# Kernel optimization log

Measured on AMD Instinct MI355X. Metric: run time of the kernel, lower is better.

The kernel has to match this reference:

```python
import jax, jax.numpy as jnp
import numpy as np
from jax import lax

DN = ('NCHW', 'OIHW', 'NCHW')
NUM_HEADS = 6


def _conv1x1(x, w):
    return lax.conv_general_dilated(x, w, (1, 1), 'VALID', dimension_numbers=DN)


def _dwconv3x3(x, w):
    # depthwise 3x3, groups == channels, padding 1
    return lax.conv_general_dilated(x, w, (1, 1), ((1, 1), (1, 1)),
                                    dimension_numbers=DN,
                                    feature_group_count=w.shape[0])


def setup_inputs() -> dict:
    key = jax.random.key(0)
    ks = jax.random.split(key, 7)
    b, dim, h, w = 4, 192, 128, 128
    inp = {
        'x': jax.random.normal(ks[0], (b, dim, h, w), jnp.float32),
        'ref': jax.random.normal(ks[1], (b, dim, h, w), jnp.float32),
        'w_qkv': jax.random.normal(ks[2], (dim * 3, dim, 1, 1), jnp.float32) * 0.05,
        'w_dw': jax.random.normal(ks[3], (dim * 3, 1, 3, 3), jnp.float32) * 0.1,
        'w_proj': jax.random.normal(ks[4], (dim, dim, 1, 1), jnp.float32) * 0.05,
        'temperature': jnp.ones((NUM_HEADS, 1, 1), jnp.float32),
        'attn_w': 0.2 * jnp.ones((4,), jnp.float32),
    }
    return inp


def reference(x, ref, w_qkv, w_dw, w_proj, temperature, attn_w):
    b, c, h, w = x.shape
    heads = NUM_HEADS
    C = c // heads  # per-head channel dim
    hw = h * w

    qkv = _dwconv3x3(_conv1x1(x, w_qkv), w_dw)        # [b, 3c, h, w]
    ref_qkv = _dwconv3x3(_conv1x1(ref, w_qkv), w_dw)  # shared weights

    q_shared = qkv[:, :c]            # q from x
    k_shared = ref_qkv[:, c:2 * c]   # k from ref
    v_shared = ref_qkv[:, 2 * c:]    # v from ref

    def to_heads(t):  # [b, c, h, w] -> [b, head, C, hw]
        return t.reshape(b, heads, C, hw)

    q = to_heads(q_shared)
    k = to_heads(k_shared)
    v = to_heads(v_shared)

    # L2-normalize along token dim (last axis)
    q = q / jnp.maximum(jnp.linalg.norm(q, axis=-1, keepdims=True), 1e-12)
    k = k / jnp.maximum(jnp.linalg.norm(k, axis=-1, keepdims=True), 1e-12)

    # channel-wise attention: [b, head, C, C]
    attn = jnp.einsum('bhcn,bhdn->bhcd', q, k) * temperature

    ks_list = [int(C / 2), int(C * 2 / 3), int(C * 3 / 4), int(C * 4 / 5)]
    neg_inf = jnp.asarray(-jnp.inf, attn.dtype)

    out = 0.0
    for i, ki in enumerate(ks_list):
        vals = lax.top_k(attn, ki)[0]            # [b, head, C, ki]
        thr = vals[..., -1:]                     # k-th largest per row
        a = jnp.where(attn >= thr, attn, neg_inf)
        a = jax.nn.softmax(a, axis=-1)
        out = out + attn_w[i] * jnp.einsum('bhcd,bhdn->bhcn', a, v)

    out = out.reshape(b, c, h, w)
    return _conv1x1(out, w_proj)
```

## Files before the change

kernel.cpp:

```cpp
#include <hip/hip_runtime.h>
#include <cstdint>
#include <cstddef>

typedef unsigned short u16;
typedef unsigned int u32;
typedef __attribute__((ext_vector_type(2))) float f32x2;
typedef __attribute__((ext_vector_type(4))) float f32x4;
typedef __attribute__((ext_vector_type(8))) short short8;
typedef __attribute__((ext_vector_type(2))) u32 u32x2;
typedef __attribute__((ext_vector_type(4))) u32 u32x4;

#define DEV static __device__ __forceinline__
#define HW 16384

DEV u16 f2bf(float f) {
  u32 u = __float_as_uint(f);
  u = (u + 0x7fffu + ((u >> 16) & 1u)) >> 16;
  return (u16)u;
}
DEV float bf2f(u16 h) { return __uint_as_float(((u32)h) << 16); }

DEV u32 packsplit(float f) {
  u16 h = f2bf(f);
  u16 l = f2bf(f - bf2f(h));
  return (u32)h | ((u32)l << 16);
}
DEV void unpack8(const u32* w, short8& hi, short8& lo) {
  #pragma unroll
  for (int i = 0; i < 8; ++i) {
    hi[i] = (short)(u16)w[i];
    lo[i] = (short)(u16)(w[i] >> 16);
  }
}
DEV void split8(const float* p, short8& hi, short8& lo) {
  f32x4 v0 = *(const f32x4*)p;
  f32x4 v1 = *(const f32x4*)(p + 4);
  #pragma unroll
  for (int j = 0; j < 4; ++j) {
    u16 h0 = f2bf(v0[j]);
    hi[j] = (short)h0; lo[j] = (short)f2bf(v0[j] - bf2f(h0));
    u16 h1 = f2bf(v1[j]);
    hi[4 + j] = (short)h1; lo[4 + j] = (short)f2bf(v1[j] - bf2f(h1));
  }
}
DEV void mfma3(f32x4& acc, short8 ah, short8 al, short8 bh, short8 bl) {
  acc = __builtin_amdgcn_mfma_f32_16x16x32_bf16(ah, bh, acc, 0, 0, 0);
  acc = __builtin_amdgcn_mfma_f32_16x16x32_bf16(ah, bl, acc, 0, 0, 0);
  acc = __builtin_amdgcn_mfma_f32_16x16x32_bf16(al, bh, acc, 0, 0, 0);
}

__global__ __launch_bounds__(256) void ksplit(const float* __restrict__ in,
                                              u32* __restrict__ out, int n) {
  int i = blockIdx.x * 256 + threadIdx.x;
  if (i < n) out[i] = packsplit(in[i]);
}

template<int ABATCH>
__global__ __launch_bounds__(512, 4) void gemm2(const u32* __restrict__ Asp,
                                                const float* __restrict__ B,
                                                float* __restrict__ C) {
  __shared__ u32 As[192 * 34];
  __shared__ u32 Bs[64 * 34];
  const int t = threadIdx.x, lane = t & 63, wid = t >> 6;
  const int b = blockIdx.z, n0 = blockIdx.x * 64;
  const u32* Ab = ABATCH ? (Asp + (size_t)b * 192 * 192) : Asp;
  const float* Bb = B + (size_t)b * 192 * (size_t)HW;
  float* Cb = C + (size_t)b * 192 * (size_t)HW;
  const int wr = wid >> 2, wc = wid & 3;
  const int g = lane >> 4, r16 = lane & 15;
  const int b_n = (t & 15) * 4, b_k = t >> 4;
  f32x4 acc[6] = {};

  f32x4 Breg, Bnext;
  u32x4 Areg[3];
  Breg = *(const f32x4*)&Bb[(size_t)b_k * HW + n0 + b_n];
  #pragma unroll
  for (int i = 0; i < 3; ++i) {
    int vi = t + i * 512;
    Areg[i] = *(const u32x4*)&Ab[(size_t)(vi >> 3) * 192 + ((vi & 7) << 2)];
  }
  #pragma unroll 1
  for (int p = 0; p < 6; ++p) {
    #pragma unroll
    for (int j = 0; j < 4; ++j)
      Bs[(b_n + j) * 34 + b_k] = packsplit(Breg[j]);
    #pragma unroll
    for (int i = 0; i < 3; ++i) {
      int vi = t + i * 512;
      int row = vi >> 3, kc = (vi & 7) << 2;
      u32x2 v0 = {Areg[i][0], Areg[i][1]};
      u32x2 v1 = {Areg[i][2], Areg[i][3]};
      *(u32x2*)&As[row * 34 + kc] = v0;
      *(u32x2*)&As[row * 34 + kc + 2] = v1;
    }
    if (p < 5)
      Bnext = *(const f32x4*)&Bb[(size_t)((p + 1) * 32 + b_k) * HW + n0 + b_n];
    __syncthreads();
    if (p < 5) {
      #pragma unroll
      for (int i = 0; i < 3; ++i) {
        int vi = t + i * 512;
        Areg[i] = *(const u32x4*)&Ab[(size_t)(vi >> 3) * 192 + (p + 1) * 32 + ((vi & 7) << 2)];
      }
    }
    u32 bw[8];
    {
      const u32* bp = &Bs[(wc * 16 + r16) * 34 + g * 8];
      *(u32x2*)&bw[0] = *(const u32x2*)&bp[0];
      *(u32x2*)&bw[2] = *(const u32x2*)&bp[2];
      *(u32x2*)&bw[4] = *(const u32x2*)&bp[4];
      *(u32x2*)&bw[6] = *(const u32x2*)&bp[6];
    }
    short8 bh, bl; unpack8(bw, bh, bl);
    #pragma unroll
    for (int mf = 0; mf < 6; ++mf) {
      u32 aw[8];
      const u32* ap = &As[(wr * 96 + mf * 16 + r16) * 34 + g * 8];
      *(u32x2*)&aw[0] = *(const u32x2*)&ap[0];
      *(u32x2*)&aw[2] = *(const u32x2*)&ap[2];
      *(u32x2*)&aw[4] = *(const u32x2*)&ap[4];
      *(u32x2*)&aw[6] = *(const u32x2*)&ap[6];
      short8 ah, al; unpack8(aw, ah, al);
      acc[mf] = __builtin_amdgcn_mfma_f32_16x16x32_bf16(ah, bh, acc[mf], 0, 0, 0);
      acc[mf] = __builtin_amdgcn_mfma_f32_16x16x32_bf16(ah, bl, acc[mf], 0, 0, 0);
      acc[mf] = __builtin_amdgcn_mfma_f32_16x16x32_bf16(al, bh, acc[mf], 0, 0, 0);
    }
    __syncthreads();
    Breg = Bnext;
  }
  #pragma unroll
  for (int mf = 0; mf < 6; ++mf)
    #pragma unroll
    for (int rr = 0; rr < 4; ++rr)
      Cb[(size_t)(wr * 96 + mf * 16 + g * 4 + rr) * HW + n0 + wc * 16 + r16] =
          acc[mf][rr];
}

template<int SSQ>
__global__ __launch_bounds__(512) void k2_dw(const float* __restrict__ Tin,
                                             const float* __restrict__ wdw, int wco,
                                             float* __restrict__ O,
                                             float* __restrict__ ssq, int sspath) {
  const int rt = blockIdx.x, cg = blockIdx.y, b = blockIdx.z;
  const int t = threadIdx.x, lane = t & 63, w = t >> 6;
  __shared__ float In[8][10][132];
  for (int idx = t; idx < 10400; idx += 512) {
    int ch = idx / 1300, rem = idx % 1300;
    int r = rem / 130, ci = rem % 130;
    int gr = rt * 8 + r - 1, gc = ci - 1;
    float v = 0.f;
    if (gr >= 0 && gr < 128 && gc >= 0 && gc < 128)
      v = Tin[((size_t)b * 192 + cg * 8 + ch) * HW + gr * 128 + gc];
    In[ch][r][ci] = v;
  }
  float wv[9];
  #pragma unroll
  for (int j = 0; j < 9; ++j) wv[j] = wdw[(size_t)(wco + cg * 8 + w) * 9 + j];
  __syncthreads();
  float s = 0.f;
  float* Op = O + ((size_t)b * 192 + cg * 8 + w) * HW + rt * 8 * 128 + 2 * lane;
  #pragma unroll
  for (int i = 0; i < 8; ++i) {
    float a0 = 0.f, a1 = 0.f;
    #pragma unroll
    for (int dr = 0; dr < 3; ++dr) {
      f32x2 u0 = *(const f32x2*)&In[w][i + dr][2 * lane];
      f32x2 u1 = *(const f32x2*)&In[w][i + dr][2 * lane + 2];
      a0 += wv[dr * 3] * u0[0] + wv[dr * 3 + 1] * u0[1] + wv[dr * 3 + 2] * u1[0];
      a1 += wv[dr * 3] * u0[1] + wv[dr * 3 + 1] * u1[0] + wv[dr * 3 + 2] * u1[1];
    }
    f32x2 o = {a0, a1};
    *(f32x2*)&Op[(size_t)i * 128] = o;
    if (SSQ) s += a0 * a0 + a1 * a1;
  }
  if (SSQ) {
    #pragma unroll
    for (int off = 32; off; off >>= 1) s += __shfl_down(s, off);
    if (lane == 0) ssq[(((size_t)b * 2 + sspath) * 192 + cg * 8 + w) * 16 + rt] = s;
  }
}

__global__ __launch_bounds__(256) void k3_gram(const float* __restrict__ q,
                                               const float* __restrict__ k,
                                               float* __restrict__ gp) {
  const int ck = blockIdx.x, bh = blockIdx.y;
  const int b = bh / 6, h = bh % 6;
  const int t = threadIdx.x, lane = t & 63, wid = t >> 6;
  const int r16 = lane & 15, g = lane >> 4;
  const int chunk = ck * 4 + wid;
  const size_t rbase = ((size_t)b * 192 + h * 32 + r16) * HW;
  const float* qp = q + rbase;
  const float* kp = k + rbase;
  f32x4 acc[2][2] = {};
  #pragma unroll 1
  for (int s = 0; s < 8; ++s) {
    int n = chunk * 256 + s * 32 + g * 8;
    short8 a0h, a0l, a1h, a1l, b0h, b0l, b1h, b1l;
    split8(&qp[n], a0h, a0l);
    split8(&qp[(size_t)16 * HW + n], a1h, a1l);
    split8(&kp[n], b0h, b0l);
    split8(&kp[(size_t)16 * HW + n], b1h, b1l);
    mfma3(acc[0][0], a0h, a0l, b0h, b0l);
    mfma3(acc[0][1], a0h, a0l, b1h, b1l);
    mfma3(acc[1][0], a1h, a1l, b0h, b0l);
    mfma3(acc[1][1], a1h, a1l, b1h, b1l);
  }
  float* outp = gp + ((size_t)bh * 64 + chunk) * 1024;
  #pragma unroll
  for (int mf = 0; mf < 2; ++mf)
    #pragma unroll
    for (int nf = 0; nf < 2; ++nf)
      #pragma unroll
      for (int rr = 0; rr < 4; ++rr)
        outp[(mf * 16 + g * 4 + rr) * 32 + nf * 16 + r16] = acc[mf][nf][rr];
}

__global__ __launch_bounds__(256) void k4_comb(const float* __restrict__ gp,
                                               const float* __restrict__ ssq,
                                               const float* __restrict__ temp,
                                               const float* __restrict__ aw,
                                               const float* __restrict__ wproj,
                                               float* __restrict__ mc) {
  const int bh = blockIdx.x, b = bh / 6, h = bh % 6;
  const int t = threadIdx.x;
  __shared__ float Gs[1024];
  __shared__ float Acm[1024];
  __shared__ float nq[32], nk[32];
  for (int e = t; e < 1024; e += 256) {
    const float* p = gp + ((size_t)bh * 64) * 1024 + e;
    float s = 0.f;
    for (int ch = 0; ch < 64; ++ch) s += p[(size_t)ch * 1024];
    Gs[e] = s;
  }
  if (t < 64) {
    int c = t & 31, pk = t >> 5;
    const float* sp = ssq + (((size_t)b * 2 + pk) * 192 + h * 32 + c) * 16;
    float s = 0.f;
    #pragma unroll
    for (int i = 0; i < 16; ++i) s += sp[i];
    float nr = fmaxf(sqrtf(s), 1e-12f);
    if (pk == 0) nq[c] = nr; else nk[c] = nr;
  }
  __syncthreads();
  const float T = temp[h];
  for (int e = t; e < 1024; e += 256) {
    int c = e >> 5, d = e & 31;
    Gs[e] = Gs[e] * T / (nq[c] * nk[d]);
  }
  __syncthreads();
  const float aw0 = aw[0], aw1 = aw[1], aw2 = aw[2], aw3 = aw[3];
  const int half = t >> 5, d = t & 31;
  for (int it = 0; it < 4; ++it) {
    const int c = it * 8 + half;
    const float v = Gs[c * 32 + d];
    int cnt = 0;
    #pragma unroll
    for (int dd = 0; dd < 32; ++dd) cnt += (Gs[c * 32 + dd] >= v) ? 1 : 0;
    float c0 = v;
    float c1 = (cnt >= 16) ? v : -3.0e38f;
    float c2 = (cnt >= 21) ? v : -3.0e38f;
    float c3 = (cnt >= 24) ? v : -3.0e38f;
    float c4 = (cnt >= 25) ? v : -3.0e38f;
    #pragma unroll
    for (int off = 16; off; off >>= 1) {
      c0 = fmaxf(c0, __shfl_xor(c0, off));
      c1 = fmaxf(c1, __shfl_xor(c1, off));
      c2 = fmaxf(c2, __shfl_xor(c2, off));
      c3 = fmaxf(c3, __shfl_xor(c3, off));
      c4 = fmaxf(c4, __shfl_xor(c4, off));
    }
    const float m = c0;
    const float ex = expf(v - m);
    float z1 = (v >= c1) ? ex : 0.f;
    float z2 = (v >= c2) ? ex : 0.f;
    float z3 = (v >= c3) ? ex : 0.f;
    float z4 = (v >= c4) ? ex : 0.f;
    #pragma unroll
    for (int off = 16; off; off >>= 1) {
      z1 += __shfl_xor(z1, off);
      z2 += __shfl_xor(z2, off);
      z3 += __shfl_xor(z3, off);
      z4 += __shfl_xor(z4, off);
    }
    float a = 0.f;
    a += (v >= c1) ? aw0 * ex / z1 : 0.f;
    a += (v >= c2) ? aw1 * ex / z2 : 0.f;
    a += (v >= c3) ? aw2 * ex / z3 : 0.f;
    a += (v >= c4) ? aw3 * ex / z4 : 0.f;
    Acm[c * 32 + d] = a;
  }
  __syncthreads();
  for (int idx = t; idx < 192 * 32; idx += 256) {
    int co = idx >> 5, dd = idx & 31;
    const float* wp = wproj + (size_t)co * 192 + h * 32;
    float s = 0.f;
    #pragma unroll
    for (int c = 0; c < 32; ++c) s += wp[c] * Acm[c * 32 + dd];
    mc[((size_t)b * 192 + co) * 192 + h * 32 + dd] = s;
  }
}

extern "C" void kernel_launch(void* const* d_in, const int* in_sizes, int n_in,
                              void* d_out, int out_size, void* d_ws, size_t ws_size,
                              hipStream_t stream) {
  const float* x     = (const float*)d_in[0];
  const float* ref   = (const float*)d_in[1];
  const float* wqkv  = (const float*)d_in[2];
  const float* wdw   = (const float*)d_in[3];
  const float* wproj = (const float*)d_in[4];
  const float* temp  = (const float*)d_in[5];
  const float* aw    = (const float*)d_in[6];
  float* out = (float*)d_out;
  char* ws = (char*)d_ws;

  const size_t S = (size_t)4 * 192 * HW * 4;
  float* tA  = (float*)(ws);
  float* tB  = (float*)(ws + S);
  float* qb  = (float*)(ws + 2 * S);
  float* kb  = (float*)(ws + 3 * S);
  float* gp  = (float*)(ws + 4 * S);
  float* ssq = (float*)(ws + 4 * S + 6291456);
  float* mc  = (float*)(ws + 4 * S + 6291456 + 98304);
  u32*   wsp = (u32*)(ws + 4 * S + 6291456 + 98304 + 589824);
  u32*   mcp = (u32*)(ws + 4 * S + 6291456 + 98304 + 589824 + 442368);

  ksplit<<<dim3(432), 256, 0, stream>>>(wqkv, wsp, 576 * 192);
  gemm2<0><<<dim3(256, 1, 4), 512, 0, stream>>>(wsp, x, tA);
  gemm2<0><<<dim3(256, 1, 4), 512, 0, stream>>>(wsp + 192 * 192, ref, tB);
  k2_dw<1><<<dim3(16, 24, 4), 512, 0, stream>>>(tA, wdw, 0, qb, ssq, 0);
  k2_dw<1><<<dim3(16, 24, 4), 512, 0, stream>>>(tB, wdw, 192, kb, ssq, 1);
  k3_gram<<<dim3(16, 24), 256, 0, stream>>>(qb, kb, gp);
  gemm2<0><<<dim3(256, 1, 4), 512, 0, stream>>>(wsp + 384 * 192, ref, tA);
  k2_dw<0><<<dim3(16, 24, 4), 512, 0, stream>>>(tA, wdw, 384, tB, nullptr, 2);
  k4_comb<<<dim3(24), 256, 0, stream>>>(gp, ssq, temp, aw, wproj, mc);
  ksplit<<<dim3(576), 256, 0, stream>>>(mc, mcp, 4 * 192 * 192);
  gemm2<1><<<dim3(256, 1, 4), 512, 0, stream>>>(mcp, tB, out);
}
```

Measured before the change: 245.3 us.

## Emit pre-split bf16 hi/lo pairs from depthwise conv and fold partial reductions

The depthwise conv now writes q, k and v as packed bf16 hi/lo pairs, so the Gram kernel and final projection GEMM read ready-made MFMA operands instead of re-splitting fp32 values. The Gram kernel reduces its four wave partials in shared memory, which cuts the partial-sum buffer and the work k4_comb does to combine it. k4_comb writes the split projection matrix directly, removing the separate ksplit launch. Launch order is also interleaved. The split is done once per element instead of in every consumer, at the cost of extra pack work inside the conv kernel.

```diff
diff --git a/kernel.cpp b/kernel.cpp
--- a/kernel.cpp
+++ b/kernel.cpp
@@ -32,17 +32,6 @@
     lo[i] = (short)(u16)(w[i] >> 16);
   }
 }
-DEV void split8(const float* p, short8& hi, short8& lo) {
-  f32x4 v0 = *(const f32x4*)p;
-  f32x4 v1 = *(const f32x4*)(p + 4);
-  #pragma unroll
-  for (int j = 0; j < 4; ++j) {
-    u16 h0 = f2bf(v0[j]);
-    hi[j] = (short)h0; lo[j] = (short)f2bf(v0[j] - bf2f(h0));
-    u16 h1 = f2bf(v1[j]);
-    hi[4 + j] = (short)h1; lo[4 + j] = (short)f2bf(v1[j] - bf2f(h1));
-  }
-}
 DEV void mfma3(f32x4& acc, short8 ah, short8 al, short8 bh, short8 bl) {
   acc = __builtin_amdgcn_mfma_f32_16x16x32_bf16(ah, bh, acc, 0, 0, 0);
   acc = __builtin_amdgcn_mfma_f32_16x16x32_bf16(ah, bl, acc, 0, 0, 0);
@@ -55,25 +44,25 @@
   if (i < n) out[i] = packsplit(in[i]);
 }
 
-template<int ABATCH>
+template<int ABATCH, int BPACKED>
 __global__ __launch_bounds__(512, 4) void gemm2(const u32* __restrict__ Asp,
-                                                const float* __restrict__ B,
+                                                const u32* __restrict__ B,
                                                 float* __restrict__ C) {
   __shared__ u32 As[192 * 34];
   __shared__ u32 Bs[64 * 34];
   const int t = threadIdx.x, lane = t & 63, wid = t >> 6;
   const int b = blockIdx.z, n0 = blockIdx.x * 64;
   const u32* Ab = ABATCH ? (Asp + (size_t)b * 192 * 192) : Asp;
-  const float* Bb = B + (size_t)b * 192 * (size_t)HW;
+  const u32* Bb = B + (size_t)b * 192 * (size_t)HW;
   float* Cb = C + (size_t)b * 192 * (size_t)HW;
   const int wr = wid >> 2, wc = wid & 3;
   const int g = lane >> 4, r16 = lane & 15;
   const int b_n = (t & 15) * 4, b_k = t >> 4;
   f32x4 acc[6] = {};
 
-  f32x4 Breg, Bnext;
+  u32x4 Breg, Bnext;
   u32x4 Areg[3];
-  Breg = *(const f32x4*)&Bb[(size_t)b_k * HW + n0 + b_n];
+  Breg = *(const u32x4*)&Bb[(size_t)b_k * HW + n0 + b_n];
   #pragma unroll
   for (int i = 0; i < 3; ++i) {
     int vi = t + i * 512;
@@ -83,7 +72,7 @@
   for (int p = 0; p < 6; ++p) {
     #pragma unroll
     for (int j = 0; j < 4; ++j)
-      Bs[(b_n + j) * 34 + b_k] = packsplit(Breg[j]);
+      Bs[(b_n + j) * 34 + b_k] = BPACKED ? Breg[j] : packsplit(__uint_as_float(Breg[j]));
     #pragma unroll
     for (int i = 0; i < 3; ++i) {
       int vi = t + i * 512;
@@ -94,7 +83,7 @@
       *(u32x2*)&As[row * 34 + kc + 2] = v1;
     }
     if (p < 5)
-      Bnext = *(const f32x4*)&Bb[(size_t)((p + 1) * 32 + b_k) * HW + n0 + b_n];
+      Bnext = *(const u32x4*)&Bb[(size_t)((p + 1) * 32 + b_k) * HW + n0 + b_n];
     __syncthreads();
     if (p < 5) {
       #pragma unroll
@@ -139,7 +128,7 @@
 template<int SSQ>
 __global__ __launch_bounds__(512) void k2_dw(const float* __restrict__ Tin,
                                              const float* __restrict__ wdw, int wco,
-                                             float* __restrict__ O,
+                                             u32* __restrict__ O,
                                              float* __restrict__ ssq, int sspath) {
   const int rt = blockIdx.x, cg = blockIdx.y, b = blockIdx.z;
   const int t = threadIdx.x, lane = t & 63, w = t >> 6;
@@ -158,7 +147,7 @@
   for (int j = 0; j < 9; ++j) wv[j] = wdw[(size_t)(wco + cg * 8 + w) * 9 + j];
   __syncthreads();
   float s = 0.f;
-  float* Op = O + ((size_t)b * 192 + cg * 8 + w) * HW + rt * 8 * 128 + 2 * lane;
+  u32* Op = O + ((size_t)b * 192 + cg * 8 + w) * HW + rt * 8 * 128 + 2 * lane;
   #pragma unroll
   for (int i = 0; i < 8; ++i) {
     float a0 = 0.f, a1 = 0.f;
@@ -169,8 +158,8 @@
       a0 += wv[dr * 3] * u0[0] + wv[dr * 3 + 1] * u0[1] + wv[dr * 3 + 2] * u1[0];
       a1 += wv[dr * 3] * u0[1] + wv[dr * 3 + 1] * u1[0] + wv[dr * 3 + 2] * u1[1];
     }
-    f32x2 o = {a0, a1};
-    *(f32x2*)&Op[(size_t)i * 128] = o;
+    u32x2 o = {packsplit(a0), packsplit(a1)};
+    *(u32x2*)&Op[(size_t)i * 128] = o;
     if (SSQ) s += a0 * a0 + a1 * a1;
   }
   if (SSQ) {
@@ -180,8 +169,8 @@
   }
 }
 
-__global__ __launch_bounds__(256) void k3_gram(const float* __restrict__ q,
-                                               const float* __restrict__ k,
+__global__ __launch_bounds__(256) void k3_gram(const u32* __restrict__ q,
+                                               const u32* __restrict__ k,
                                                float* __restrict__ gp) {
   const int ck = blockIdx.x, bh = blockIdx.y;
   const int b = bh / 6, h = bh % 6;
@@ -189,30 +178,44 @@
   const int r16 = lane & 15, g = lane >> 4;
   const int chunk = ck * 4 + wid;
   const size_t rbase = ((size_t)b * 192 + h * 32 + r16) * HW;
-  const float* qp = q + rbase;
-  const float* kp = k + rbase;
+  const u32* qp = q + rbase;
+  const u32* kp = k + rbase;
+  __shared__ float red[4][1024];
   f32x4 acc[2][2] = {};
   #pragma unroll 1
   for (int s = 0; s < 8; ++s) {
     int n = chunk * 256 + s * 32 + g * 8;
+    u32 wq0[8], wq1[8], wk0[8], wk1[8];
+    *(u32x4*)&wq0[0] = *(const u32x4*)&qp[n];
+    *(u32x4*)&wq0[4] = *(const u32x4*)&qp[n + 4];
+    *(u32x4*)&wq1[0] = *(const u32x4*)&qp[(size_t)16 * HW + n];
+    *(u32x4*)&wq1[4] = *(const u32x4*)&qp[(size_t)16 * HW + n + 4];
+    *(u32x4*)&wk0[0] = *(const u32x4*)&kp[n];
+    *(u32x4*)&wk0[4] = *(const u32x4*)&kp[n + 4];
+    *(u32x4*)&wk1[0] = *(const u32x4*)&kp[(size_t)16 * HW + n];
+    *(u32x4*)&wk1[4] = *(const u32x4*)&kp[(size_t)16 * HW + n + 4];
     short8 a0h, a0l, a1h, a1l, b0h, b0l, b1h, b1l;
-    split8(&qp[n], a0h, a0l);
-    split8(&qp[(size_t)16 * HW + n], a1h, a1l);
-    split8(&kp[n], b0h, b0l);
-    split8(&kp[(size_t)16 * HW + n], b1h, b1l);
+    unpack8(wq0, a0h, a0l);
+    unpack8(wq1, a1h, a1l);
+    unpack8(wk0, b0h, b0l);
+    unpack8(wk1, b1h, b1l);
     mfma3(acc[0][0], a0h, a0l, b0h, b0l);
     mfma3(acc[0][1], a0h, a0l, b1h, b1l);
     mfma3(acc[1][0], a1h, a1l, b0h, b0l);
     mfma3(acc[1][1], a1h, a1l, b1h, b1l);
   }
-  float* outp = gp + ((size_t)bh * 64 + chunk) * 1024;
   #pragma unroll
   for (int mf = 0; mf < 2; ++mf)
     #pragma unroll
     for (int nf = 0; nf < 2; ++nf)
       #pragma unroll
       for (int rr = 0; rr < 4; ++rr)
-        outp[(mf * 16 + g * 4 + rr) * 32 + nf * 16 + r16] = acc[mf][nf][rr];
+        red[wid][(mf * 16 + g * 4 + rr) * 32 + nf * 16 + r16] = acc[mf][nf][rr];
+  __syncthreads();
+  float* outp = gp + ((size_t)bh * 16 + ck) * 1024;
+  #pragma unroll
+  for (int e = t; e < 1024; e += 256)
+    outp[e] = red[0][e] + red[1][e] + red[2][e] + red[3][e];
 }
 
 __global__ __launch_bounds__(256) void k4_comb(const float* __restrict__ gp,
@@ -220,17 +223,21 @@
                                                const float* __restrict__ temp,
                                                const float* __restrict__ aw,
                                                const float* __restrict__ wproj,
-                                               float* __restrict__ mc) {
+                                               u32* __restrict__ mcp) {
   const int bh = blockIdx.x, b = bh / 6, h = bh % 6;
   const int t = threadIdx.x;
   __shared__ float Gs[1024];
   __shared__ float Acm[1024];
   __shared__ float nq[32], nk[32];
-  for (int e = t; e < 1024; e += 256) {
-    const float* p = gp + ((size_t)bh * 64) * 1024 + e;
-    float s = 0.f;
-    for (int ch = 0; ch < 64; ++ch) s += p[(size_t)ch * 1024];
-    Gs[e] = s;
+  {
+    const float* p = gp + (size_t)bh * 16 * 1024 + 4 * t;
+    f32x4 s = {};
+    #pragma unroll
+    for (int ch = 0; ch < 16; ++ch) {
+      f32x4 v = *(const f32x4*)&p[(size_t)ch * 1024];
+      s[0] += v[0]; s[1] += v[1]; s[2] += v[2]; s[3] += v[3];
+    }
+    *(f32x4*)&Gs[4 * t] = s;
   }
   if (t < 64) {
     int c = t & 31, pk = t >> 5;
@@ -296,7 +303,7 @@
     float s = 0.f;
     #pragma unroll
     for (int c = 0; c < 32; ++c) s += wp[c] * Acm[c * 32 + dd];
-    mc[((size_t)b * 192 + co) * 192 + h * 32 + dd] = s;
+    mcp[((size_t)b * 192 + co) * 192 + h * 32 + dd] = packsplit(s);
   }
 }
 
@@ -316,23 +323,22 @@
   const size_t S = (size_t)4 * 192 * HW * 4;
   float* tA  = (float*)(ws);
   float* tB  = (float*)(ws + S);
-  float* qb  = (float*)(ws + 2 * S);
-  float* kb  = (float*)(ws + 3 * S);
+  u32*   qpk = (u32*)(ws + 2 * S);
+  u32*   kpk = (u32*)(ws + 3 * S);
   float* gp  = (float*)(ws + 4 * S);
-  float* ssq = (float*)(ws + 4 * S + 6291456);
-  float* mc  = (float*)(ws + 4 * S + 6291456 + 98304);
-  u32*   wsp = (u32*)(ws + 4 * S + 6291456 + 98304 + 589824);
-  u32*   mcp = (u32*)(ws + 4 * S + 6291456 + 98304 + 589824 + 442368);
+  float* ssq = (float*)(ws + 4 * S + 1572864);
+  u32*   wsp = (u32*)(ws + 4 * S + 1572864 + 98304);
+  u32*   mcp = (u32*)(ws + 4 * S + 1572864 + 98304 + 442368);
+  u32*   vpk = (u32*)tB;
 
   ksplit<<<dim3(432), 256, 0, stream>>>(wqkv, wsp, 576 * 192);
-  gemm2<0><<<dim3(256, 1, 4), 512, 0, stream>>>(wsp, x, tA);
-  gemm2<0><<<dim3(256, 1, 4), 512, 0, stream>>>(wsp + 192 * 192, ref, tB);
-  k2_dw<1><<<dim3(16, 24, 4), 512, 0, stream>>>(tA, wdw, 0, qb, ssq, 0);
-  k2_dw<1><<<dim3(16, 24, 4), 512, 0, stream>>>(tB, wdw, 192, kb, ssq, 1);
-  k3_gram<<<dim3(16, 24), 256, 0, stream>>>(qb, kb, gp);
-  gemm2<0><<<dim3(256, 1, 4), 512, 0, stream>>>(wsp + 384 * 192, ref, tA);
-  k2_dw<0><<<dim3(16, 24, 4), 512, 0, stream>>>(tA, wdw, 384, tB, nullptr, 2);
-  k4_comb<<<dim3(24), 256, 0, stream>>>(gp, ssq, temp, aw, wproj, mc);
-  ksplit<<<dim3(576), 256, 0, stream>>>(mc, mcp, 4 * 192 * 192);
-  gemm2<1><<<dim3(256, 1, 4), 512, 0, stream>>>(mcp, tB, out);
-}
+  gemm2<0, 0><<<dim3(256, 1, 4), 512, 0, stream>>>(wsp, (const u32*)x, tA);
+  k2_dw<1><<<dim3(16, 24, 4), 512, 0, stream>>>(tA, wdw, 0, qpk, ssq, 0);
+  gemm2<0, 0><<<dim3(256, 1, 4), 512, 0, stream>>>(wsp + 192 * 192, (const u32*)ref, tB);
+  k2_dw<1><<<dim3(16, 24, 4), 512, 0, stream>>>(tB, wdw, 192, kpk, ssq, 1);
+  k3_gram<<<dim3(16, 24), 256, 0, stream>>>(qpk, kpk, gp);
+  gemm2<0, 0><<<dim3(256, 1, 4), 512, 0, stream>>>(wsp + 384 * 192, (const u32*)ref, tA);
+  k2_dw<0><<<dim3(16, 24, 4), 512, 0, stream>>>(tA, wdw, 384, vpk, nullptr, 2);
+  k4_comb<<<dim3(24), 256, 0, stream>>>(gp, ssq, temp, aw, wproj, mcp);
+  gemm2<1, 1><<<dim3(256, 1, 4), 512, 0, stream>>>(mcp, vpk, out);
+}
```

Result: no change. 240.9 us (-1.8%).
